# Kernel optimization log

Measured on AMD Instinct MI355X. Metric: run time of the kernel, lower is better.

## Reference

```python
import jax, jax.numpy as jnp
import numpy as np

B, T, D, U = 64, 2048, 512, 512

def setup_inputs() -> dict:
    key = jax.random.key(0)
    ks = jax.random.split(key, 5)
    scale = 1.0 / np.sqrt(D)
    return {
        "query": jax.random.normal(ks[0], (B, D), dtype=jnp.float32),
        "values": jax.random.normal(ks[1], (B, T, D), dtype=jnp.float32),
        "W1": jax.random.normal(ks[2], (D, U), dtype=jnp.float32) * scale,
        "b1": jnp.zeros((U,), dtype=jnp.float32),
        "W2": jax.random.normal(ks[3], (D, U), dtype=jnp.float32) * scale,
        "b2": jnp.zeros((U,), dtype=jnp.float32),
        "Wv": jax.random.normal(ks[4], (U, 1), dtype=jnp.float32) * (1.0 / np.sqrt(U)),
        "bv": jnp.zeros((1,), dtype=jnp.float32),
    }

def reference(query, values, W1, b1, W2, b2, Wv, bv):
    # mask: True where the timestep has any nonzero feature -> [B, T, 1]
    mask = ~jnp.all(values == 0, axis=-1, keepdims=True)
    # query gets a broadcast time axis: [B, 1, U]
    q_proj = query @ W1 + b1                       # [B, U]
    v_proj = jnp.einsum('btd,du->btu', values, W2) + b2  # [B, T, U]
    hidden = jnp.tanh(q_proj[:, None, :] + v_proj)       # [B, T, U]
    score = hidden @ Wv + bv                       # [B, T, 1]
    score = jnp.where(mask, score, -jnp.inf)
    attention_weights = jax.nn.softmax(score, axis=1)    # [B, T, 1]
    # matmul(attn^T, values) -> [B, 1, D]; reduce_sum over axis=1 -> [B, D]
    context_vector = jnp.einsum('bt,btd->bd', attention_weights[..., 0], values)
    return context_vector, attention_weights
```

## Files before the change

kernel.cpp:

```cpp
#include <hip/hip_runtime.h>
#include <hip/hip_bf16.h>
#include <math.h>

#define B_ 64
#define T_ 2048
#define D_ 512
#define U_ 512

typedef __attribute__((ext_vector_type(8))) short short8;
typedef __attribute__((ext_vector_type(4))) float f32x4;

__device__ __forceinline__ unsigned short f2bf(float x) {
  unsigned int u = __float_as_uint(x);
  unsigned int r = u + 0x7fffu + ((u >> 16) & 1u);
  return (unsigned short)(r >> 16);
}

__device__ __forceinline__ float tanh_fast(float x) {
  float e = __expf(2.f * x);
  return 1.f - 2.f * __builtin_amdgcn_rcpf(e + 1.f);
}

#define SWZ(off, rc) ((off) ^ ((unsigned)((rc) & 7) << 4))

__global__ __launch_bounds__(256) void k_qproj(const float* __restrict__ query,
                                               const float* __restrict__ W1,
                                               const float* __restrict__ b1,
                                               float* __restrict__ qproj) {
  const int b = blockIdx.x;
  const int tid = threadIdx.x;
  __shared__ float q[D_];
  q[tid] = query[b * D_ + tid];
  q[tid + 256] = query[b * D_ + tid + 256];
  __syncthreads();
  float a0 = 0.f, a1 = 0.f;
#pragma unroll 8
  for (int d = 0; d < D_; d++) {
    float qd = q[d];
    a0 = fmaf(qd, W1[d * U_ + tid], a0);
    a1 = fmaf(qd, W1[d * U_ + tid + 256], a1);
  }
  qproj[b * U_ + tid] = a0 + b1[tid];
  qproj[b * U_ + tid + 256] = a1 + b1[tid + 256];
}

__global__ __launch_bounds__(256) void k_w2t(const float* __restrict__ W2,
                                             unsigned short* __restrict__ w2t) {
  __shared__ float tile[32][33];
  const int k0 = blockIdx.y * 32, u0 = blockIdx.x * 32;
  const int tx = threadIdx.x, ty = threadIdx.y;
#pragma unroll
  for (int r = 0; r < 4; r++)
    tile[ty + 8 * r][tx] = W2[(size_t)(k0 + ty + 8 * r) * U_ + (u0 + tx)];
  __syncthreads();
#pragma unroll
  for (int r = 0; r < 4; r++) {
    int u_l = ty + 8 * r, k_l = tx;
    w2t[(size_t)(u0 + u_l) * D_ + (k0 + k_l)] = f2bf(tile[k_l][u_l]);
  }
}

__global__ __launch_bounds__(512, 4) void k_score(
    const float* __restrict__ values, const unsigned short* __restrict__ w2t,
    const float* __restrict__ qproj, const float* __restrict__ b2,
    const float* __restrict__ Wv, const float* __restrict__ bv,
    float* __restrict__ scores) {
  __shared__ __align__(16) unsigned short lsA[64 * 64];
  __shared__ __align__(16) unsigned short lsB[U_ * 64];
  __shared__ float qp[U_];
  __shared__ float wv_s[U_];
  __shared__ float red[64 * 8];
  __shared__ int rowflag[64];

  const int tid = threadIdx.x;
  const int wid = tid >> 6;
  const int lane = tid & 63;
  const int m0 = blockIdx.x * 64;
  const int b = m0 >> 11;

  qp[tid] = qproj[b * U_ + tid] + b2[tid];
  wv_s[tid] = Wv[tid];
  if (tid < 64) rowflag[tid] = 0;

  const int arow = tid >> 3;
  const int akq = tid & 7;
  const float* aptr = values + (size_t)(m0 + arow) * D_ + akq * 8;
  char* lsAc = (char*)lsA;
  char* lsBc = (char*)lsB;
  const unsigned int aoff = SWZ((unsigned)(arow * 128 + akq * 16), arow);

  f32x4 acc[4][4];
#pragma unroll
  for (int i = 0; i < 4; i++)
#pragma unroll
    for (int j = 0; j < 4; j++) acc[i][j] = (f32x4){0.f, 0.f, 0.f, 0.f};

  const int colbase = wid * 64;
  __syncthreads();

  for (int kk = 0; kk < D_; kk += 64) {
#pragma unroll
    for (int r = 0; r < 8; r++) {
      unsigned int off = (unsigned)tid * 16 + (unsigned)r * 8192;
      unsigned int col = off >> 7;
      unsigned int logical = off ^ ((col & 7u) << 4);
      unsigned int klocal = (logical & 127u) >> 1;
      const unsigned short* src = w2t + (size_t)col * D_ + kk + klocal;
      __builtin_amdgcn_global_load_lds(
          (const __attribute__((address_space(1))) unsigned int*)src,
          (__attribute__((address_space(3))) unsigned int*)(lsBc + (size_t)wid * 1024 + (size_t)r * 8192),
          16, 0, 0);
    }
    float4 v0 = *(const float4*)(aptr + kk);
    float4 v1 = *(const float4*)(aptr + kk + 4);
    if (v0.x != 0.f || v0.y != 0.f || v0.z != 0.f || v0.w != 0.f ||
        v1.x != 0.f || v1.y != 0.f || v1.z != 0.f || v1.w != 0.f)
      rowflag[arow] = 1;
    uint4 pk;
    pk.x = (unsigned)f2bf(v0.x) | ((unsigned)f2bf(v0.y) << 16);
    pk.y = (unsigned)f2bf(v0.z) | ((unsigned)f2bf(v0.w) << 16);
    pk.z = (unsigned)f2bf(v1.x) | ((unsigned)f2bf(v1.y) << 16);
    pk.w = (unsigned)f2bf(v1.z) | ((unsigned)f2bf(v1.w) << 16);
    *(uint4*)(lsAc + aoff) = pk;

    __syncthreads();

#pragma unroll
    for (int kh = 0; kh < 2; kh++) {
      short8 af[4], bf[4];
#pragma unroll
      for (int fr = 0; fr < 4; fr++) {
        int row = fr * 16 + (lane & 15);
        unsigned int lg = (unsigned)(row * 128 + kh * 64 + (lane >> 4) * 16);
        af[fr] = *(const short8*)(lsAc + SWZ(lg, row));
      }
#pragma unroll
      for (int fc = 0; fc < 4; fc++) {
        int col = colbase + fc * 16 + (lane & 15);
        unsigned int lg = (unsigned)(col * 128 + kh * 64 + (lane >> 4) * 16);
        bf[fc] = *(const short8*)(lsBc + SWZ(lg, col));
      }
#pragma unroll
      for (int fr = 0; fr < 4; fr++)
#pragma unroll
        for (int fc = 0; fc < 4; fc++)
          acc[fr][fc] = __builtin_amdgcn_mfma_f32_16x16x32_bf16(af[fr], bf[fc], acc[fr][fc], 0, 0, 0);
    }
    __syncthreads();
  }

  const int rgrp = lane >> 4;
  const int cl = lane & 15;
  float ps[4][4];
#pragma unroll
  for (int fr = 0; fr < 4; fr++)
#pragma unroll
    for (int r = 0; r < 4; r++) ps[fr][r] = 0.f;

#pragma unroll
  for (int fc = 0; fc < 4; fc++) {
    int u = colbase + fc * 16 + cl;
    float qpu = qp[u], wvu = wv_s[u];
#pragma unroll
    for (int fr = 0; fr < 4; fr++)
#pragma unroll
      for (int r = 0; r < 4; r++)
        ps[fr][r] = fmaf(tanh_fast(acc[fr][fc][r] + qpu), wvu, ps[fr][r]);
  }
#pragma unroll
  for (int fr = 0; fr < 4; fr++)
#pragma unroll
    for (int r = 0; r < 4; r++) {
      float v = ps[fr][r];
      v += __shfl_xor(v, 1, 64);
      v += __shfl_xor(v, 2, 64);
      v += __shfl_xor(v, 4, 64);
      v += __shfl_xor(v, 8, 64);
      if (cl == 0) red[(fr * 16 + rgrp * 4 + r) * 8 + wid] = v;
    }
  __syncthreads();
  if (tid < 64) {
    float s = bv[0];
#pragma unroll
    for (int w = 0; w < 8; w++) s += red[tid * 8 + w];
    if (!rowflag[tid]) s = -INFINITY;
    scores[m0 + tid] = s;
  }
}

__global__ __launch_bounds__(256) void k_softmax(const float* __restrict__ scores,
                                                 float* __restrict__ attn) {
  const int b = blockIdx.x, tid = threadIdx.x;
  const float* srow = scores + (size_t)b * T_;
  float s[8];
  float m = -INFINITY;
#pragma unroll
  for (int j = 0; j < 8; j++) {
    s[j] = srow[tid + 256 * j];
    m = fmaxf(m, s[j]);
  }
#pragma unroll
  for (int o = 1; o < 64; o <<= 1) m = fmaxf(m, __shfl_xor(m, o, 64));
  __shared__ float redm[4], redsum[4];
  if ((tid & 63) == 0) redm[tid >> 6] = m;
  __syncthreads();
  m = fmaxf(fmaxf(redm[0], redm[1]), fmaxf(redm[2], redm[3]));
  float sum = 0.f;
#pragma unroll
  for (int j = 0; j < 8; j++) {
    s[j] = __expf(s[j] - m);
    sum += s[j];
  }
#pragma unroll
  for (int o = 1; o < 64; o <<= 1) sum += __shfl_xor(sum, o, 64);
  if ((tid & 63) == 0) redsum[tid >> 6] = sum;
  __syncthreads();
  sum = redsum[0] + redsum[1] + redsum[2] + redsum[3];
  float inv = 1.f / sum;
#pragma unroll
  for (int j = 0; j < 8; j++) attn[(size_t)b * T_ + tid + 256 * j] = s[j] * inv;
}

__global__ __launch_bounds__(128) void k_ctx_part(const float* __restrict__ values,
                                                  const float* __restrict__ attn,
                                                  float* __restrict__ part) {
  const int tc = blockIdx.x, b = blockIdx.y;
  const int tid = threadIdx.x;
  const float4* vp = (const float4*)(values + ((size_t)b * T_ + tc * 128) * D_);
  const float* ap = attn + (size_t)b * T_ + tc * 128;
  float4 acc = {0.f, 0.f, 0.f, 0.f};
#pragma unroll 4
  for (int t = 0; t < 128; t++) {
    float w = ap[t];
    float4 v = vp[(size_t)t * 128 + tid];
    acc.x = fmaf(w, v.x, acc.x);
    acc.y = fmaf(w, v.y, acc.y);
    acc.z = fmaf(w, v.z, acc.z);
    acc.w = fmaf(w, v.w, acc.w);
  }
  float4* pp = (float4*)(part + (size_t)(b * 16 + tc) * D_);
  pp[tid] = acc;
}

__global__ __launch_bounds__(256) void k_ctx_reduce(const float* __restrict__ part,
                                                    float* __restrict__ ctx) {
  const int gid = blockIdx.x * 256 + threadIdx.x;
  const int b = gid >> 9, d = gid & 511;
  float s = 0.f;
#pragma unroll
  for (int tc = 0; tc < 16; tc++) s += part[(size_t)(b * 16 + tc) * D_ + d];
  ctx[gid] = s;
}

extern "C" void kernel_launch(void* const* d_in, const int* in_sizes, int n_in,
                              void* d_out, int out_size, void* d_ws, size_t ws_size,
                              hipStream_t stream) {
  const float* query  = (const float*)d_in[0];
  const float* values = (const float*)d_in[1];
  const float* W1     = (const float*)d_in[2];
  const float* b1     = (const float*)d_in[3];
  const float* W2     = (const float*)d_in[4];
  const float* b2     = (const float*)d_in[5];
  const float* Wv     = (const float*)d_in[6];
  const float* bv     = (const float*)d_in[7];

  float* out_ctx = (float*)d_out;
  float* out_attn = out_ctx + B_ * D_;

  char* ws = (char*)d_ws;
  float* qproj          = (float*)ws;
  unsigned short* w2t   = (unsigned short*)(ws + (128 << 10));
  float* scores         = (float*)(ws + (640 << 10));
  float* part           = (float*)(ws + (1152 << 10));

  k_qproj<<<dim3(B_), dim3(256), 0, stream>>>(query, W1, b1, qproj);
  k_w2t<<<dim3(16, 16), dim3(32, 8), 0, stream>>>(W2, w2t);
  k_score<<<dim3((B_ * T_) / 64), dim3(512), 0, stream>>>(values, w2t, qproj, b2, Wv, bv, scores);
  k_softmax<<<dim3(B_), dim3(256), 0, stream>>>(scores, out_attn);
  k_ctx_part<<<dim3(16, B_), dim3(128), 0, stream>>>(values, out_attn, part);
  k_ctx_reduce<<<dim3(128), dim3(256), 0, stream>>>(part, out_ctx);
}
```

Measured before the change: 189.1 us.

## Double-buffer LDS tiles with K=32 steps and overlap global loads with MFMA

The score GEMM loop now uses two LDS buffers with 32-wide K slices in place of one 64-wide slice. Next-tile global loads (direct-to-LDS for W2 and register loads for values) are issued before the current tile's MFMAs, and explicit vmcnt/lgkmcnt waits replace full syncthreads. A new XOR swizzle suited to the 64-byte rows is added. The goal is to hide memory latency behind compute, at the cost of twice as many barriers and fragile hand-written waitcnt ordering.

Result: slower. 207.6 us (+9.8%).

```diff
diff --git a/kernel.cpp b/kernel.cpp
--- a/kernel.cpp
+++ b/kernel.cpp
@@ -10,10 +10,10 @@
 typedef __attribute__((ext_vector_type(8))) short short8;
 typedef __attribute__((ext_vector_type(4))) float f32x4;
 
-__device__ __forceinline__ unsigned short f2bf(float x) {
+__device__ __forceinline__ unsigned int f2bf(float x) {
   unsigned int u = __float_as_uint(x);
   unsigned int r = u + 0x7fffu + ((u >> 16) & 1u);
-  return (unsigned short)(r >> 16);
+  return r >> 16;
 }
 
 __device__ __forceinline__ float tanh_fast(float x) {
@@ -21,7 +21,7 @@
   return 1.f - 2.f * __builtin_amdgcn_rcpf(e + 1.f);
 }
 
-#define SWZ(off, rc) ((off) ^ ((unsigned)((rc) & 7) << 4))
+__device__ __forceinline__ unsigned swz4(unsigned rc) { return (rc + (rc >> 2)) & 3u; }
 
 __global__ __launch_bounds__(256) void k_qproj(const float* __restrict__ query,
                                                const float* __restrict__ W1,
@@ -56,8 +56,17 @@
 #pragma unroll
   for (int r = 0; r < 4; r++) {
     int u_l = ty + 8 * r, k_l = tx;
-    w2t[(size_t)(u0 + u_l) * D_ + (k0 + k_l)] = f2bf(tile[k_l][u_l]);
-  }
+    w2t[(size_t)(u0 + u_l) * D_ + (k0 + k_l)] = (unsigned short)f2bf(tile[k_l][u_l]);
+  }
+}
+
+__device__ __forceinline__ void storeA(char* bufA, float4 av, unsigned awoff,
+                                       int* rowflag, int arow) {
+  if (av.x != 0.f || av.y != 0.f || av.z != 0.f || av.w != 0.f) rowflag[arow] = 1;
+  uint2 pk;
+  pk.x = f2bf(av.x) | (f2bf(av.y) << 16);
+  pk.y = f2bf(av.z) | (f2bf(av.w) << 16);
+  *(uint2*)(bufA + awoff) = pk;
 }
 
 __global__ __launch_bounds__(512, 4) void k_score(
@@ -65,8 +74,8 @@
     const float* __restrict__ qproj, const float* __restrict__ b2,
     const float* __restrict__ Wv, const float* __restrict__ bv,
     float* __restrict__ scores) {
-  __shared__ __align__(16) unsigned short lsA[64 * 64];
-  __shared__ __align__(16) unsigned short lsB[U_ * 64];
+  __shared__ __align__(16) unsigned short lsA[2][64 * 32];
+  __shared__ __align__(16) unsigned short lsB[2][512 * 32];
   __shared__ float qp[U_];
   __shared__ float wv_s[U_];
   __shared__ float red[64 * 8];
@@ -83,11 +92,18 @@
   if (tid < 64) rowflag[tid] = 0;
 
   const int arow = tid >> 3;
-  const int akq = tid & 7;
-  const float* aptr = values + (size_t)(m0 + arow) * D_ + akq * 8;
+  const int achunk = tid & 7;
+  const float* aptr = values + (size_t)(m0 + arow) * D_ + achunk * 4;
+  const unsigned awoff = (unsigned)(arow * 64) +
+                         ((((unsigned)achunk >> 1) ^ swz4((unsigned)arow)) << 4) +
+                         ((unsigned)(achunk & 1) << 3);
+
+  const int bcol0 = tid >> 2;
+  const unsigned bs = (unsigned)(tid & 3);
+
   char* lsAc = (char*)lsA;
   char* lsBc = (char*)lsB;
-  const unsigned int aoff = SWZ((unsigned)(arow * 128 + akq * 16), arow);
+  const int colbase = wid * 64;
 
   f32x4 acc[4][4];
 #pragma unroll
@@ -95,58 +111,93 @@
 #pragma unroll
     for (int j = 0; j < 4; j++) acc[i][j] = (f32x4){0.f, 0.f, 0.f, 0.f};
 
-  const int colbase = wid * 64;
-  __syncthreads();
-
-  for (int kk = 0; kk < D_; kk += 64) {
-#pragma unroll
-    for (int r = 0; r < 8; r++) {
-      unsigned int off = (unsigned)tid * 16 + (unsigned)r * 8192;
-      unsigned int col = off >> 7;
-      unsigned int logical = off ^ ((col & 7u) << 4);
-      unsigned int klocal = (logical & 127u) >> 1;
-      const unsigned short* src = w2t + (size_t)col * D_ + kk + klocal;
+  asm volatile("s_waitcnt vmcnt(0)" ::: "memory");
+
+  float4 av = *(const float4*)aptr;
+  asm volatile("" ::: "memory");
+#pragma unroll
+  for (int r = 0; r < 4; r++) {
+    int col = bcol0 + r * 128;
+    const unsigned short* src = w2t + (size_t)col * D_ + ((bs ^ swz4((unsigned)col)) << 3);
+    __builtin_amdgcn_global_load_lds(
+        (const __attribute__((address_space(1))) unsigned int*)src,
+        (__attribute__((address_space(3))) unsigned int*)(lsBc + wid * 1024 + r * 8192),
+        16, 0, 0);
+  }
+  asm volatile("s_waitcnt vmcnt(4)" ::: "memory");
+  storeA(lsAc, av, awoff, rowflag, arow);
+  asm volatile("s_waitcnt lgkmcnt(0)" ::: "memory");
+  __builtin_amdgcn_s_barrier();
+
+#pragma unroll 1
+  for (int t = 0; t < 15; t++) {
+    char* curA = lsAc + (t & 1) * 4096;
+    char* curB = lsBc + (t & 1) * 32768;
+    char* nxtA = lsAc + ((t + 1) & 1) * 4096;
+    char* nxtB = lsBc + ((t + 1) & 1) * 32768;
+    const int kk = (t + 1) * 32;
+
+    float4 av2 = *(const float4*)(aptr + kk);
+    asm volatile("" ::: "memory");
+#pragma unroll
+    for (int r = 0; r < 4; r++) {
+      int col = bcol0 + r * 128;
+      const unsigned short* src =
+          w2t + (size_t)col * D_ + kk + ((bs ^ swz4((unsigned)col)) << 3);
       __builtin_amdgcn_global_load_lds(
           (const __attribute__((address_space(1))) unsigned int*)src,
-          (__attribute__((address_space(3))) unsigned int*)(lsBc + (size_t)wid * 1024 + (size_t)r * 8192),
+          (__attribute__((address_space(3))) unsigned int*)(nxtB + wid * 1024 + r * 8192),
           16, 0, 0);
     }
-    float4 v0 = *(const float4*)(aptr + kk);
-    float4 v1 = *(const float4*)(aptr + kk + 4);
-    if (v0.x != 0.f || v0.y != 0.f || v0.z != 0.f || v0.w != 0.f ||
-        v1.x != 0.f || v1.y != 0.f || v1.z != 0.f || v1.w != 0.f)
-      rowflag[arow] = 1;
-    uint4 pk;
-    pk.x = (unsigned)f2bf(v0.x) | ((unsigned)f2bf(v0.y) << 16);
-    pk.y = (unsigned)f2bf(v0.z) | ((unsigned)f2bf(v0.w) << 16);
-    pk.z = (unsigned)f2bf(v1.x) | ((unsigned)f2bf(v1.y) << 16);
-    pk.w = (unsigned)f2bf(v1.z) | ((unsigned)f2bf(v1.w) << 16);
-    *(uint4*)(lsAc + aoff) = pk;
-
-    __syncthreads();
-
-#pragma unroll
-    for (int kh = 0; kh < 2; kh++) {
-      short8 af[4], bf[4];
-#pragma unroll
-      for (int fr = 0; fr < 4; fr++) {
-        int row = fr * 16 + (lane & 15);
-        unsigned int lg = (unsigned)(row * 128 + kh * 64 + (lane >> 4) * 16);
-        af[fr] = *(const short8*)(lsAc + SWZ(lg, row));
-      }
-#pragma unroll
-      for (int fc = 0; fc < 4; fc++) {
-        int col = colbase + fc * 16 + (lane & 15);
-        unsigned int lg = (unsigned)(col * 128 + kh * 64 + (lane >> 4) * 16);
-        bf[fc] = *(const short8*)(lsBc + SWZ(lg, col));
-      }
-#pragma unroll
-      for (int fr = 0; fr < 4; fr++)
-#pragma unroll
-        for (int fc = 0; fc < 4; fc++)
-          acc[fr][fc] = __builtin_amdgcn_mfma_f32_16x16x32_bf16(af[fr], bf[fc], acc[fr][fc], 0, 0, 0);
-    }
-    __syncthreads();
+    asm volatile("s_waitcnt vmcnt(5)" ::: "memory");
+
+    short8 af[4], bf[4];
+#pragma unroll
+    for (int fr = 0; fr < 4; fr++) {
+      int row = fr * 16 + (lane & 15);
+      af[fr] = *(const short8*)(curA + row * 64 +
+                                ((((unsigned)lane >> 4) ^ swz4((unsigned)row)) << 4));
+    }
+#pragma unroll
+    for (int fc = 0; fc < 4; fc++) {
+      int col = colbase + fc * 16 + (lane & 15);
+      bf[fc] = *(const short8*)(curB + col * 64 +
+                                ((((unsigned)lane >> 4) ^ swz4((unsigned)col)) << 4));
+    }
+#pragma unroll
+    for (int fr = 0; fr < 4; fr++)
+#pragma unroll
+      for (int fc = 0; fc < 4; fc++)
+        acc[fr][fc] = __builtin_amdgcn_mfma_f32_16x16x32_bf16(af[fr], bf[fc], acc[fr][fc], 0, 0, 0);
+
+    asm volatile("s_waitcnt vmcnt(4)" ::: "memory");
+    storeA(nxtA, av2, awoff, rowflag, arow);
+    asm volatile("s_waitcnt lgkmcnt(0)" ::: "memory");
+    __builtin_amdgcn_s_barrier();
+  }
+
+  asm volatile("s_waitcnt vmcnt(0)" ::: "memory");
+  {
+    char* curA = lsAc + 4096;
+    char* curB = lsBc + 32768;
+    short8 af[4], bf[4];
+#pragma unroll
+    for (int fr = 0; fr < 4; fr++) {
+      int row = fr * 16 + (lane & 15);
+      af[fr] = *(const short8*)(curA + row * 64 +
+                                ((((unsigned)lane >> 4) ^ swz4((unsigned)row)) << 4));
+    }
+#pragma unroll
+    for (int fc = 0; fc < 4; fc++) {
+      int col = colbase + fc * 16 + (lane & 15);
+      bf[fc] = *(const short8*)(curB + col * 64 +
+                                ((((unsigned)lane >> 4) ^ swz4((unsigned)col)) << 4));
+    }
+#pragma unroll
+    for (int fr = 0; fr < 4; fr++)
+#pragma unroll
+      for (int fc = 0; fc < 4; fc++)
+        acc[fr][fc] = __builtin_amdgcn_mfma_f32_16x16x32_bf16(af[fr], bf[fc], acc[fr][fc], 0, 0, 0);
   }
 
   const int rgrp = lane >> 4;
```

## Double-buffer LDS tiles in score GEMM to overlap loads with MFMA

Applied to the files above, without the earlier changes.

Splits the A and B shared-memory tiles into two buffers and prefetches the next K-slice (async global_load_lds for W2^T, register loads for values) while MFMAs run on the current slice. This drops one barrier per iteration and hides global load latency behind compute. LDS use roughly doubles to about 145KB, so the launch bound drops from 4 to 2 blocks per SM and occupancy falls, which could offset the gain.

Result: slower. 255.8 us (+35.3%).

```diff
diff --git a/kernel.cpp b/kernel.cpp
--- a/kernel.cpp
+++ b/kernel.cpp
@@ -10,10 +10,10 @@
 typedef __attribute__((ext_vector_type(8))) short short8;
 typedef __attribute__((ext_vector_type(4))) float f32x4;
 
-__device__ __forceinline__ unsigned short f2bf(float x) {
+__device__ __forceinline__ unsigned int f2bf(float x) {
   unsigned int u = __float_as_uint(x);
   unsigned int r = u + 0x7fffu + ((u >> 16) & 1u);
-  return (unsigned short)(r >> 16);
+  return r >> 16;
 }
 
 __device__ __forceinline__ float tanh_fast(float x) {
@@ -56,17 +56,17 @@
 #pragma unroll
   for (int r = 0; r < 4; r++) {
     int u_l = ty + 8 * r, k_l = tx;
-    w2t[(size_t)(u0 + u_l) * D_ + (k0 + k_l)] = f2bf(tile[k_l][u_l]);
-  }
-}
-
-__global__ __launch_bounds__(512, 4) void k_score(
+    w2t[(size_t)(u0 + u_l) * D_ + (k0 + k_l)] = (unsigned short)f2bf(tile[k_l][u_l]);
+  }
+}
+
+__global__ __launch_bounds__(512, 2) void k_score(
     const float* __restrict__ values, const unsigned short* __restrict__ w2t,
     const float* __restrict__ qproj, const float* __restrict__ b2,
     const float* __restrict__ Wv, const float* __restrict__ bv,
     float* __restrict__ scores) {
-  __shared__ __align__(16) unsigned short lsA[64 * 64];
-  __shared__ __align__(16) unsigned short lsB[U_ * 64];
+  __shared__ __align__(16) unsigned short lsA[2][64 * 64];
+  __shared__ __align__(16) unsigned short lsB[2][U_ * 64];
   __shared__ float qp[U_];
   __shared__ float wv_s[U_];
   __shared__ float red[64 * 8];
@@ -87,7 +87,7 @@
   const float* aptr = values + (size_t)(m0 + arow) * D_ + akq * 8;
   char* lsAc = (char*)lsA;
   char* lsBc = (char*)lsB;
-  const unsigned int aoff = SWZ((unsigned)(arow * 128 + akq * 16), arow);
+  const unsigned aoff = SWZ((unsigned)(arow * 128 + akq * 16), arow);
 
   f32x4 acc[4][4];
 #pragma unroll
@@ -96,34 +96,60 @@
     for (int j = 0; j < 4; j++) acc[i][j] = (f32x4){0.f, 0.f, 0.f, 0.f};
 
   const int colbase = wid * 64;
-  __syncthreads();
-
-  for (int kk = 0; kk < D_; kk += 64) {
+
+  {
+    float4 v0 = *(const float4*)aptr;
+    float4 v1 = *(const float4*)(aptr + 4);
 #pragma unroll
     for (int r = 0; r < 8; r++) {
       unsigned int off = (unsigned)tid * 16 + (unsigned)r * 8192;
       unsigned int col = off >> 7;
       unsigned int logical = off ^ ((col & 7u) << 4);
       unsigned int klocal = (logical & 127u) >> 1;
-      const unsigned short* src = w2t + (size_t)col * D_ + kk + klocal;
+      const unsigned short* src = w2t + (size_t)col * D_ + klocal;
       __builtin_amdgcn_global_load_lds(
           (const __attribute__((address_space(1))) unsigned int*)src,
           (__attribute__((address_space(3))) unsigned int*)(lsBc + (size_t)wid * 1024 + (size_t)r * 8192),
           16, 0, 0);
     }
-    float4 v0 = *(const float4*)(aptr + kk);
-    float4 v1 = *(const float4*)(aptr + kk + 4);
     if (v0.x != 0.f || v0.y != 0.f || v0.z != 0.f || v0.w != 0.f ||
         v1.x != 0.f || v1.y != 0.f || v1.z != 0.f || v1.w != 0.f)
       rowflag[arow] = 1;
     uint4 pk;
-    pk.x = (unsigned)f2bf(v0.x) | ((unsigned)f2bf(v0.y) << 16);
-    pk.y = (unsigned)f2bf(v0.z) | ((unsigned)f2bf(v0.w) << 16);
-    pk.z = (unsigned)f2bf(v1.x) | ((unsigned)f2bf(v1.y) << 16);
-    pk.w = (unsigned)f2bf(v1.z) | ((unsigned)f2bf(v1.w) << 16);
+    pk.x = f2bf(v0.x) | (f2bf(v0.y) << 16);
+    pk.y = f2bf(v0.z) | (f2bf(v0.w) << 16);
+    pk.z = f2bf(v1.x) | (f2bf(v1.y) << 16);
+    pk.w = f2bf(v1.z) | (f2bf(v1.w) << 16);
     *(uint4*)(lsAc + aoff) = pk;
-
-    __syncthreads();
+  }
+  __syncthreads();
+
+#pragma unroll 1
+  for (int t = 0; t < 8; t++) {
+    char* curA = lsAc + (t & 1) * 8192;
+    char* curB = lsBc + (t & 1) * 65536;
+    char* nxtA = lsAc + ((t + 1) & 1) * 8192;
+    char* nxtB = lsBc + ((t + 1) & 1) * 65536;
+
+    float4 v0, v1;
+    if (t < 7) {
+      const int kk = (t + 1) * 64;
+      v0 = *(const float4*)(aptr + kk);
+      v1 = *(const float4*)(aptr + kk + 4);
+#pragma unroll
+      for (int r = 0; r < 8; r++) {
+        unsigned int off = (unsigned)tid * 16 + (unsigned)r * 8192;
+        unsigned int col = off >> 7;
+        unsigned int logical = off ^ ((col & 7u) << 4);
+        unsigned int klocal = (logical & 127u) >> 1;
+        const unsigned short* src = w2t + (size_t)col * D_ + kk + klocal;
+        __builtin_amdgcn_global_load_lds(
+            (const __attribute__((address_space(1))) unsigned int*)src,
+            (__attribute__((address_space(3))) unsigned int*)(nxtB + (size_t)wid * 1024 + (size_t)r * 8192),
+            16, 0, 0);
+      }
+    }
+    asm volatile("" ::: "memory");
 
 #pragma unroll
     for (int kh = 0; kh < 2; kh++) {
@@ -132,19 +158,31 @@
       for (int fr = 0; fr < 4; fr++) {
         int row = fr * 16 + (lane & 15);
         unsigned int lg = (unsigned)(row * 128 + kh * 64 + (lane >> 4) * 16);
-        af[fr] = *(const short8*)(lsAc + SWZ(lg, row));
+        af[fr] = *(const short8*)(curA + SWZ(lg, row));
       }
 #pragma unroll
       for (int fc = 0; fc < 4; fc++) {
         int col = colbase + fc * 16 + (lane & 15);
         unsigned int lg = (unsigned)(col * 128 + kh * 64 + (lane >> 4) * 16);
-        bf[fc] = *(const short8*)(lsBc + SWZ(lg, col));
+        bf[fc] = *(const short8*)(curB + SWZ(lg, col));
       }
 #pragma unroll
       for (int fr = 0; fr < 4; fr++)
 #pragma unroll
         for (int fc = 0; fc < 4; fc++)
           acc[fr][fc] = __builtin_amdgcn_mfma_f32_16x16x32_bf16(af[fr], bf[fc], acc[fr][fc], 0, 0, 0);
+    }
+
+    if (t < 7) {
+      if (v0.x != 0.f || v0.y != 0.f || v0.z != 0.f || v0.w != 0.f ||
+          v1.x != 0.f || v1.y != 0.f || v1.z != 0.f || v1.w != 0.f)
+        rowflag[arow] = 1;
+      uint4 pk;
+      pk.x = f2bf(v0.x) | (f2bf(v0.y) << 16);
+      pk.y = f2bf(v0.z) | (f2bf(v0.w) << 16);
+      pk.z = f2bf(v1.x) | (f2bf(v1.y) << 16);
+      pk.w = f2bf(v1.z) | (f2bf(v1.w) << 16);
+      *(uint4*)(nxtA + aoff) = pk;
     }
     __syncthreads();
   }
```

## Stage whole A tile in LDS once and stream pre-packed W2 fragments from global

Applied to the files above, without the earlier changes.

The score kernel now loads and converts the block's full 64x512 values tile into LDS in one pass, with a new swizzle and a single barrier. It no longer stages the whole W2 slice into LDS on every k-step; each wave reads B fragments directly from a W2 copy pre-packed in MFMA fragment order, expected to hit in L2. qproj and Wv are kept in registers, and the row mask is computed from the packed bf16 bits with a shuffle-OR. This removes per-iteration barriers and the large LDS B copy, at the cost of 64KB of LDS per block, which limits occupancy. It also drops the bv bias, which only shifts every score by the same constant and leaves the softmax unchanged.

Result: slower. 202.3 us (+7.0%).

```diff
diff --git a/kernel.cpp b/kernel.cpp
--- a/kernel.cpp
+++ b/kernel.cpp
@@ -6,22 +6,21 @@
 #define T_ 2048
 #define D_ 512
 #define U_ 512
+#define NT_ (B_ * T_)
 
 typedef __attribute__((ext_vector_type(8))) short short8;
 typedef __attribute__((ext_vector_type(4))) float f32x4;
 
-__device__ __forceinline__ unsigned short f2bf(float x) {
+__device__ __forceinline__ unsigned int f2bf(float x) {
   unsigned int u = __float_as_uint(x);
   unsigned int r = u + 0x7fffu + ((u >> 16) & 1u);
-  return (unsigned short)(r >> 16);
+  return r >> 16;
 }
 
 __device__ __forceinline__ float tanh_fast(float x) {
   float e = __expf(2.f * x);
   return 1.f - 2.f * __builtin_amdgcn_rcpf(e + 1.f);
 }
-
-#define SWZ(off, rc) ((off) ^ ((unsigned)((rc) & 7) << 4))
 
 __global__ __launch_bounds__(256) void k_qproj(const float* __restrict__ query,
                                                const float* __restrict__ W1,
@@ -44,50 +43,75 @@
   qproj[b * U_ + tid + 256] = a1 + b1[tid + 256];
 }
 
-__global__ __launch_bounds__(256) void k_w2t(const float* __restrict__ W2,
-                                             unsigned short* __restrict__ w2t) {
-  __shared__ float tile[32][33];
-  const int k0 = blockIdx.y * 32, u0 = blockIdx.x * 32;
-  const int tx = threadIdx.x, ty = threadIdx.y;
-#pragma unroll
-  for (int r = 0; r < 4; r++)
-    tile[ty + 8 * r][tx] = W2[(size_t)(k0 + ty + 8 * r) * U_ + (u0 + tx)];
-  __syncthreads();
-#pragma unroll
-  for (int r = 0; r < 4; r++) {
-    int u_l = ty + 8 * r, k_l = tx;
-    w2t[(size_t)(u0 + u_l) * D_ + (k0 + k_l)] = f2bf(tile[k_l][u_l]);
-  }
-}
-
-__global__ __launch_bounds__(512, 4) void k_score(
-    const float* __restrict__ values, const unsigned short* __restrict__ w2t,
+__global__ __launch_bounds__(256) void k_w2t2(const float* __restrict__ W2,
+                                              unsigned short* __restrict__ w2t2) {
+  const int gid = blockIdx.x * 256 + threadIdx.x;
+  const int chunk = gid >> 6;
+  const int lane = gid & 63;
+  const int ut = chunk >> 4, kc = chunk & 15;
+  const int u = ut * 16 + (lane & 15);
+  const int k0 = kc * 32 + (lane >> 4) * 8;
+  uint4 pk;
+  unsigned p[4];
+#pragma unroll
+  for (int i = 0; i < 4; i++) {
+    float e0 = W2[(size_t)(k0 + 2 * i) * U_ + u];
+    float e1 = W2[(size_t)(k0 + 2 * i + 1) * U_ + u];
+    p[i] = f2bf(e0) | (f2bf(e1) << 16);
+  }
+  pk.x = p[0]; pk.y = p[1]; pk.z = p[2]; pk.w = p[3];
+  *(uint4*)(w2t2 + (size_t)chunk * 512 + lane * 8) = pk;
+}
+
+__global__ __launch_bounds__(512) void k_score(
+    const float* __restrict__ values, const unsigned short* __restrict__ w2t2,
     const float* __restrict__ qproj, const float* __restrict__ b2,
-    const float* __restrict__ Wv, const float* __restrict__ bv,
-    float* __restrict__ scores) {
-  __shared__ __align__(16) unsigned short lsA[64 * 64];
-  __shared__ __align__(16) unsigned short lsB[U_ * 64];
-  __shared__ float qp[U_];
-  __shared__ float wv_s[U_];
-  __shared__ float red[64 * 8];
-  __shared__ int rowflag[64];
+    const float* __restrict__ Wv, float* __restrict__ scores) {
+  __shared__ __align__(16) char pool[67840];
+  char* lsA = pool;
+  float* red = (float*)(pool + 65536);
+  int* flg = (int*)(pool + 67584);
 
   const int tid = threadIdx.x;
   const int wid = tid >> 6;
   const int lane = tid & 63;
+  const int cl = lane & 15;
+  const int kg = lane >> 4;
   const int m0 = blockIdx.x * 64;
   const int b = m0 >> 11;
 
-  qp[tid] = qproj[b * U_ + tid] + b2[tid];
-  wv_s[tid] = Wv[tid];
-  if (tid < 64) rowflag[tid] = 0;
+  float qp_r[4], wv_r[4];
+#pragma unroll
+  for (int fc = 0; fc < 4; fc++) {
+    int u = wid * 64 + fc * 16 + cl;
+    qp_r[fc] = qproj[b * U_ + u] + b2[u];
+    wv_r[fc] = Wv[u];
+  }
 
   const int arow = tid >> 3;
   const int akq = tid & 7;
-  const float* aptr = values + (size_t)(m0 + arow) * D_ + akq * 8;
-  char* lsAc = (char*)lsA;
-  char* lsBc = (char*)lsB;
-  const unsigned int aoff = SWZ((unsigned)(arow * 128 + akq * 16), arow);
+  const float* aptr = values + (size_t)(m0 + arow) * D_;
+  unsigned rfb = 0;
+#pragma unroll
+  for (int c = 0; c < 8; c++) {
+    const int k0 = c * 64 + akq * 8;
+    float4 a0 = *(const float4*)(aptr + k0);
+    float4 a1 = *(const float4*)(aptr + k0 + 4);
+    uint4 pk;
+    pk.x = f2bf(a0.x) | (f2bf(a0.y) << 16);
+    pk.y = f2bf(a0.z) | (f2bf(a0.w) << 16);
+    pk.z = f2bf(a1.x) | (f2bf(a1.y) << 16);
+    pk.w = f2bf(a1.z) | (f2bf(a1.w) << 16);
+    rfb |= pk.x | pk.y | pk.z | pk.w;
+    const int kc = k0 >> 5;
+    const int slot = akq & 3;
+    *(uint4*)(lsA + kc * 4096 + arow * 64 + ((slot ^ ((arow >> 1) & 3)) << 4)) = pk;
+  }
+  rfb |= __shfl_xor((int)rfb, 1, 64);
+  rfb |= __shfl_xor((int)rfb, 2, 64);
+  rfb |= __shfl_xor((int)rfb, 4, 64);
+  if (akq == 0) flg[arow] = (rfb != 0);
+  __syncthreads();
 
   f32x4 acc[4][4];
 #pragma unroll
@@ -95,72 +119,35 @@
 #pragma unroll
     for (int j = 0; j < 4; j++) acc[i][j] = (f32x4){0.f, 0.f, 0.f, 0.f};
 
-  const int colbase = wid * 64;
-  __syncthreads();
-
-  for (int kk = 0; kk < D_; kk += 64) {
-#pragma unroll
-    for (int r = 0; r < 8; r++) {
-      unsigned int off = (unsigned)tid * 16 + (unsigned)r * 8192;
-      unsigned int col = off >> 7;
-      unsigned int logical = off ^ ((col & 7u) << 4);
-      unsigned int klocal = (logical & 127u) >> 1;
-      const unsigned short* src = w2t + (size_t)col * D_ + kk + klocal;
-      __builtin_amdgcn_global_load_lds(
-          (const __attribute__((address_space(1))) unsigned int*)src,
-          (__attribute__((address_space(3))) unsigned int*)(lsBc + (size_t)wid * 1024 + (size_t)r * 8192),
-          16, 0, 0);
+  const char* bbase = (const char*)w2t2 + (size_t)wid * 65536 + lane * 16;
+
+#pragma unroll 2
+  for (int t = 0; t < 16; t++) {
+    short8 bf[4], af[4];
+#pragma unroll
+    for (int fc = 0; fc < 4; fc++)
+      bf[fc] = *(const short8*)(bbase + fc * 16384 + t * 1024);
+#pragma unroll
+    for (int fr = 0; fr < 4; fr++) {
+      int row = fr * 16 + cl;
+      af[fr] = *(const short8*)(lsA + t * 4096 + row * 64 +
+                                (((kg ^ ((row >> 1) & 3)) & 3) << 4));
     }
-    float4 v0 = *(const float4*)(aptr + kk);
-    float4 v1 = *(const float4*)(aptr + kk + 4);
-    if (v0.x != 0.f || v0.y != 0.f || v0.z != 0.f || v0.w != 0.f ||
-        v1.x != 0.f || v1.y != 0.f || v1.z != 0.f || v1.w != 0.f)
-      rowflag[arow] = 1;
-    uint4 pk;
-    pk.x = (unsigned)f2bf(v0.x) | ((unsigned)f2bf(v0.y) << 16);
-    pk.y = (unsigned)f2bf(v0.z) | ((unsigned)f2bf(v0.w) << 16);
-    pk.z = (unsigned)f2bf(v1.x) | ((unsigned)f2bf(v1.y) << 16);
-    pk.w = (unsigned)f2bf(v1.z) | ((unsigned)f2bf(v1.w) << 16);
-    *(uint4*)(lsAc + aoff) = pk;
-
-    __syncthreads();
-
-#pragma unroll
-    for (int kh = 0; kh < 2; kh++) {
-      short8 af[4], bf[4];
-#pragma unroll
-      for (int fr = 0; fr < 4; fr++) {
-        int row = fr * 16 + (lane & 15);
-        unsigned int lg = (unsigned)(row * 128 + kh * 64 + (lane >> 4) * 16);
-        af[fr] = *(const short8*)(lsAc + SWZ(lg, row));
-      }
-#pragma unroll
-      for (int fc = 0; fc < 4; fc++) {
-        int col = colbase + fc * 16 + (lane & 15);
-        unsigned int lg = (unsigned)(col * 128 + kh * 64 + (lane >> 4) * 16);
-        bf[fc] = *(const short8*)(lsBc + SWZ(lg, col));
-      }
-#pragma unroll
-      for (int fr = 0; fr < 4; fr++)
-#pragma unroll
-        for (int fc = 0; fc < 4; fc++)
-          acc[fr][fc] = __builtin_amdgcn_mfma_f32_16x16x32_bf16(af[fr], bf[fc], acc[fr][fc], 0, 0, 0);
-    }
-    __syncthreads();
-  }
-
-  const int rgrp = lane >> 4;
-  const int cl = lane & 15;
+#pragma unroll
+    for (int fr = 0; fr < 4; fr++)
+#pragma unroll
+      for (int fc = 0; fc < 4; fc++)
+        acc[fr][fc] = __builtin_amdgcn_mfma_f32_16x16x32_bf16(af[fr], bf[fc], acc[fr][fc], 0, 0, 0);
+  }
+
   float ps[4][4];
 #pragma unroll
   for (int fr = 0; fr < 4; fr++)
 #pragma unroll
     for (int r = 0; r < 4; r++) ps[fr][r] = 0.f;
-
 #pragma unroll
   for (int fc = 0; fc < 4; fc++) {
-    int u = colbase + fc * 16 + cl;
-    float qpu = qp[u], wvu = wv_s[u];
+    float qpu = qp_r[fc], wvu = wv_r[fc];
 #pragma unroll
     for (int fr = 0; fr < 4; fr++)
 #pragma unroll
@@ -176,14 +163,14 @@
       v += __shfl_xor(v, 2, 64);
       v += __shfl_xor(v, 4, 64);
       v += __shfl_xor(v, 8, 64);
-      if (cl == 0) red[(fr * 16 + rgrp * 4 + r) * 8 + wid] = v;
+      if (cl == 0) red[(fr * 16 + kg * 4 + r) * 8 + wid] = v;
     }
   __syncthreads();
   if (tid < 64) {
-    float s = bv[0];
+    float s = 0.f;
 #pragma unroll
     for (int w = 0; w < 8; w++) s += red[tid * 8 + w];
-    if (!rowflag[tid]) s = -INFINITY;
+    if (!flg[tid]) s = -INFINITY;
     scores[m0 + tid] = s;
   }
 }
@@ -262,20 +249,19 @@
   const float* W2     = (const float*)d_in[4];
   const float* b2     = (const float*)d_in[5];
   const float* Wv     = (const float*)d_in[6];
-  const float* bv     = (const float*)d_in[7];
 
   float* out_ctx = (float*)d_out;
   float* out_attn = out_ctx + B_ * D_;
 
   char* ws = (char*)d_ws;
   float* qproj          = (float*)ws;
-  unsigned short* w2t   = (unsigned short*)(ws + (128 << 10));
+  unsigned short* w2t2  = (unsigned short*)(ws + (128 << 10));
   float* scores         = (float*)(ws + (640 << 10));
   float* part           = (float*)(ws + (1152 << 10));
 
   k_qproj<<<dim3(B_), dim3(256), 0, stream>>>(query, W1, b1, qproj);
-  k_w2t<<<dim3(16, 16), dim3(32, 8), 0, stream>>>(W2, w2t);
-  k_score<<<dim3((B_ * T_) / 64), dim3(512), 0, stream>>>(values, w2t, qproj, b2, Wv, bv, scores);
+  k_w2t2<<<dim3(128), dim3(256), 0, stream>>>(W2, w2t2);
+  k_score<<<dim3((B_ * T_) / 64), dim3(512), 0, stream>>>(values, w2t2, qproj, b2, Wv, scores);
   k_softmax<<<dim3(B_), dim3(256), 0, stream>>>(scores, out_attn);
   k_ctx_part<<<dim3(16, B_), dim3(128), 0, stream>>>(values, out_attn, part);
   k_ctx_reduce<<<dim3(128), dim3(256), 0, stream>>>(part, out_ctx);
```
